# Kernel optimization log

Hardware: AMD Instinct MI355X
Metric: run time of the kernel (lower is better)

Reference implementation:

```python
import jax, jax.numpy as jnp
import numpy as np

EMBED_DIM = 1024
NUM_HEADS = 16


def setup_inputs() -> dict:
    key = jax.random.key(0)
    kx, kq, kk, kv, ko = jax.random.split(key, 5)
    B, S, D = 2, 2048, EMBED_DIM
    s = 1.0 / np.sqrt(D)
    return {
        "x": jax.random.normal(kx, (B, S, D), dtype=jnp.float32),
        "Wq": jax.random.normal(kq, (D, D), dtype=jnp.float32) * s,
        "Wk": jax.random.normal(kk, (D, D), dtype=jnp.float32) * s,
        "Wv": jax.random.normal(kv, (D, D), dtype=jnp.float32) * s,
        "Wo": jax.random.normal(ko, (D, D), dtype=jnp.float32) * s,
    }


def reference(x, Wq, Wk, Wv, Wo):
    B, S, D = x.shape
    H = NUM_HEADS
    d_k = D // H
    # QKV projections (nn.Linear applies x @ W.T)
    q = (x @ Wq.T).reshape(B, S, H, d_k).transpose(0, 2, 1, 3)  # [B,H,S,d_k]
    k = (x @ Wk.T).reshape(B, S, H, d_k).transpose(0, 2, 1, 3)
    v = (x @ Wv.T).reshape(B, S, H, d_k).transpose(0, 2, 1, 3)
    scores = jnp.einsum("bhqd,bhkd->bhqk", q, k) / jnp.sqrt(jnp.float32(d_k))
    probs = jax.nn.softmax(scores, axis=-1)  # dropout is identity in eval
    attn = jnp.einsum("bhqk,bhkd->bhqd", probs, v)  # [B,H,S,d_k]
    attn = attn.transpose(0, 2, 1, 3).reshape(B, S, D)
    return attn @ Wo.T
```

## Files before the change

kernel.cpp:

```cpp
#include <hip/hip_runtime.h>
#include <stdint.h>

typedef __attribute__((ext_vector_type(4))) float    f32x4;
typedef __attribute__((ext_vector_type(8))) _Float16 half8;
typedef __attribute__((ext_vector_type(4))) _Float16 half4;

#define MFMA16(a, b, c)   __builtin_amdgcn_mfma_f32_16x16x32_f16(a, b, c, 0, 0, 0)
#define MFMA16K16(a, b, c) __builtin_amdgcn_mfma_f32_16x16x16f16(a, b, c, 0, 0, 0)

#if __has_builtin(__builtin_amdgcn_exp2f)
#define EXP2F(x) __builtin_amdgcn_exp2f(x)
#else
#define EXP2F(x) exp2f(x)
#endif

#define CEXP 0.18033688f

__device__ inline void gl_lds16(const void* g, void* l) {
    __builtin_amdgcn_global_load_lds(
        (const __attribute__((address_space(1))) unsigned int*)g,
        (__attribute__((address_space(3))) unsigned int*)l, 16, 0, 0);
}

__global__ __launch_bounds__(256) void cast_all(
    const float* __restrict__ x,  const float* __restrict__ wq,
    const float* __restrict__ wk, const float* __restrict__ wv,
    const float* __restrict__ wo,
    _Float16* __restrict__ xh,  _Float16* __restrict__ wqh,
    _Float16* __restrict__ wkh, _Float16* __restrict__ wvh,
    _Float16* __restrict__ woh) {
    const int NX = 4194304, NW = 1048576;
    int i = (blockIdx.x * 256 + threadIdx.x) * 4;
    const float* src; _Float16* dst; int off;
    if (i < NX) { src = x; dst = xh; off = i; }
    else {
        int j = i - NX; int w = j >> 20; off = j & (NW - 1);
        src = (w == 0) ? wq : (w == 1) ? wk : (w == 2) ? wv : wo;
        dst = (w == 0) ? wqh : (w == 1) ? wkh : (w == 2) ? wvh : woh;
    }
    f32x4 v = *(const f32x4*)(src + off);
    half4 o;
    o.x = (_Float16)v.x; o.y = (_Float16)v.y; o.z = (_Float16)v.z; o.w = (_Float16)v.w;
    *(half4*)(dst + off) = o;
}

#define BN 128
#define BK 64

template <int MODE>
__global__ __launch_bounds__(256) void gemm_bt(const _Float16* __restrict__ A,
                                               const _Float16* __restrict__ B,
                                               void* __restrict__ C0,
                                               void* __restrict__ C1,
                                               void* __restrict__ C2,
                                               int M, int N, int K) {
    constexpr int BM  = (MODE == 3) ? 128 : 64;
    constexpr int MT  = BM / 32;
    constexpr int AIT = BM / 32;

    __shared__ __attribute__((aligned(16))) _Float16 As[BM * BK];
    __shared__ __attribute__((aligned(16))) _Float16 Bs[BN * BK];

    const int tid  = threadIdx.x;
    const int wave = tid >> 6;
    const int lane = tid & 63;
    const int l16  = lane & 15;
    const int quad = lane >> 4;
    const int m0 = blockIdx.y * BM;
    const int n0 = blockIdx.x * BN;
    const int wm = (wave >> 1) * (BM / 2);
    const int wn = (wave & 1) * 64;

    const int srow = tid >> 3;
    const int scc  = (tid & 7) ^ ((tid >> 3) & 7);

    f32x4 acc[MT][4];
#pragma unroll
    for (int i = 0; i < MT; i++)
#pragma unroll
        for (int j = 0; j < 4; j++) acc[i][j] = (f32x4){0.f, 0.f, 0.f, 0.f};

    for (int k0 = 0; k0 < K; k0 += BK) {
        __syncthreads();
#pragma unroll
        for (int i = 0; i < AIT; i++)
            gl_lds16(A + (size_t)(m0 + i * 32 + srow) * K + k0 + scc * 8,
                     (char*)As + i * 4096 + wave * 1024);
#pragma unroll
        for (int i = 0; i < 4; i++)
            gl_lds16(B + (size_t)(n0 + i * 32 + srow) * K + k0 + scc * 8,
                     (char*)Bs + i * 4096 + wave * 1024);
        __syncthreads();

#pragma unroll
        for (int kk = 0; kk < 2; kk++) {
            half8 af[MT], bf[4];
#pragma unroll
            for (int mt = 0; mt < MT; mt++) {
                int row = wm + mt * 16 + l16;
                af[mt] = *(const half8*)(As + row * 64 + ((quad + 4 * kk) ^ (row & 7)) * 8);
            }
#pragma unroll
            for (int nt = 0; nt < 4; nt++) {
                int row = wn + nt * 16 + l16;
                bf[nt] = *(const half8*)(Bs + row * 64 + ((quad + 4 * kk) ^ (row & 7)) * 8);
            }
#pragma unroll
            for (int mt = 0; mt < MT; mt++)
#pragma unroll
                for (int nt = 0; nt < 4; nt++)
                    acc[mt][nt] = MFMA16(af[mt], bf[nt], acc[mt][nt]);
        }
    }

    if (MODE == 0) {
        float* C = (float*)C0;
#pragma unroll
        for (int mt = 0; mt < MT; mt++)
#pragma unroll
            for (int r = 0; r < 4; r++) {
                int row = m0 + wm + mt * 16 + quad * 4 + r;
                float* Crow = C + (size_t)row * N + n0 + wn + l16;
#pragma unroll
                for (int nt = 0; nt < 4; nt++) Crow[nt * 16] = acc[mt][nt][r];
            }
    } else {
        const int region = n0 >> 10;
        const int nb = (n0 & 1023) + wn;
        if (region < 2) {
            _Float16* C = (region == 0) ? (_Float16*)C0 : (_Float16*)C1;
#pragma unroll
            for (int mt = 0; mt < MT; mt++)
#pragma unroll
                for (int r = 0; r < 4; r++) {
                    int mg = m0 + wm + mt * 16 + quad * 4 + r;
                    int b = mg >> 11, s = mg & 2047;
#pragma unroll
                    for (int nt = 0; nt < 4; nt++) {
                        int nw = nb + nt * 16 + l16;
                        int h = nw >> 6, d = nw & 63;
                        C[(((size_t)b * 16 + h) * 2048 + s) * 64 + d] = (_Float16)acc[mt][nt][r];
                    }
                }
        } else {
            _Float16* C = (_Float16*)C2;
#pragma unroll
            for (int mt = 0; mt < MT; mt++) {
                int mg = m0 + wm + mt * 16 + quad * 4;
                int b = mg >> 11, s = mg & 2047;
#pragma unroll
                for (int nt = 0; nt < 4; nt++) {
                    int nw = nb + nt * 16 + l16;
                    int h = nw >> 6, d = nw & 63;
                    half4 o;
#pragma unroll
                    for (int r = 0; r < 4; r++) o[r] = (_Float16)acc[mt][nt][r];
                    *(half4*)(C + (((size_t)b * 16 + h) * 64 + d) * 2048 + s) = o;
                }
            }
        }
    }
}

__global__ __launch_bounds__(256) void attn_kernel(const _Float16* __restrict__ Q,
                                                   const _Float16* __restrict__ Kg,
                                                   const _Float16* __restrict__ Vt,
                                                   _Float16* __restrict__ Oa) {
    __shared__ __attribute__((aligned(16))) _Float16 Ks[64 * 64];
    __shared__ __attribute__((aligned(16))) _Float16 Vs[64 * 64];

    const int tid  = threadIdx.x;
    const int wave = tid >> 6;
    const int lane = tid & 63;
    const int l16  = lane & 15;
    const int quad = lane >> 4;
    const int bh = blockIdx.y;
    const int q0 = blockIdx.x * 128 + wave * 32;

    half8 qf[2][2];
#pragma unroll
    for (int qt = 0; qt < 2; qt++)
#pragma unroll
        for (int kk = 0; kk < 2; kk++)
            qf[qt][kk] = *(const half8*)(Q + ((size_t)bh * 2048 + q0 + qt * 16 + l16) * 64 +
                                         (quad + 4 * kk) * 8);

    const _Float16* Kbase = Kg + (size_t)bh * 2048 * 64;
    const _Float16* Vbase = Vt + (size_t)bh * 64 * 2048;

    float lsum[2] = {0.f, 0.f};
    f32x4 oacc[2][4];
#pragma unroll
    for (int qt = 0; qt < 2; qt++)
#pragma unroll
        for (int dt = 0; dt < 4; dt++) oacc[qt][dt] = (f32x4){0.f, 0.f, 0.f, 0.f};

    const int srow = tid >> 3;
    const int scc  = (tid & 7) ^ ((tid >> 3) & 7);

    for (int kt = 0; kt < 2048; kt += 64) {
        __syncthreads();
#pragma unroll
        for (int i = 0; i < 2; i++) {
            int row = i * 32 + srow;
            gl_lds16(Kbase + (size_t)(kt + row) * 64 + scc * 8,
                     (char*)Ks + i * 4096 + wave * 1024);
            gl_lds16(Vbase + (size_t)row * 2048 + kt + scc * 8,
                     (char*)Vs + i * 4096 + wave * 1024);
        }
        __syncthreads();

        f32x4 sc4[2][4];
#pragma unroll
        for (int nt = 0; nt < 4; nt++) {
            int row = nt * 16 + l16;
            half8 kf0 = *(const half8*)(Ks + row * 64 + (quad ^ (row & 7)) * 8);
            half8 kf1 = *(const half8*)(Ks + row * 64 + ((quad + 4) ^ (row & 7)) * 8);
#pragma unroll
            for (int qt = 0; qt < 2; qt++) {
                f32x4 s = (f32x4){0.f, 0.f, 0.f, 0.f};
                s = MFMA16(kf0, qf[qt][0], s);
                s = MFMA16(kf1, qf[qt][1], s);
                sc4[qt][nt] = s;
            }
        }

        half4 ph[2][4];
#pragma unroll
        for (int qt = 0; qt < 2; qt++)
#pragma unroll
            for (int nt = 0; nt < 4; nt++) {
                half4 p;
#pragma unroll
                for (int r = 0; r < 4; r++) {
                    float pe = EXP2F(sc4[qt][nt][r] * CEXP);
                    lsum[qt] += pe;
                    p[r] = (_Float16)pe;
                }
                ph[qt][nt] = p;
            }

#pragma unroll
        for (int nt = 0; nt < 4; nt++) {
#pragma unroll
            for (int dt = 0; dt < 4; dt++) {
                int row = dt * 16 + l16;
                int ch = (nt * 2 + (quad >> 1)) ^ (row & 7);
                half4 vf = *(const half4*)(Vs + row * 64 + ch * 8 + (quad & 1) * 4);
#pragma unroll
                for (int qt = 0; qt < 2; qt++)
                    oacc[qt][dt] = MFMA16K16(vf, ph[qt][nt], oacc[qt][dt]);
            }
        }
    }

    const int b = bh >> 4, h = bh & 15;
#pragma unroll
    for (int qt = 0; qt < 2; qt++) {
        float ls = lsum[qt];
        ls += __shfl_xor(ls, 16);
        ls += __shfl_xor(ls, 32);
        float inv = 1.f / ls;
        int q = q0 + qt * 16 + l16;
        _Float16* orow = Oa + ((size_t)b * 2048 + q) * 1024 + h * 64;
#pragma unroll
        for (int dt = 0; dt < 4; dt++) {
            half4 o;
#pragma unroll
            for (int r = 0; r < 4; r++) o[r] = (_Float16)(oacc[qt][dt][r] * inv);
            *(half4*)(orow + dt * 16 + quad * 4) = o;
        }
    }
}

extern "C" void kernel_launch(void* const* d_in, const int* in_sizes, int n_in,
                              void* d_out, int out_size, void* d_ws, size_t ws_size,
                              hipStream_t stream) {
    const float* x  = (const float*)d_in[0];
    const float* Wq = (const float*)d_in[1];
    const float* Wk = (const float*)d_in[2];
    const float* Wv = (const float*)d_in[3];
    const float* Wo = (const float*)d_in[4];
    float* out = (float*)d_out;

    const int NX = 2 * 2048 * 1024;
    const int NW = 1024 * 1024;

    _Float16* ws  = (_Float16*)d_ws;
    _Float16* xh  = ws;
    _Float16* wqh = xh + NX;
    _Float16* wkh = wqh + NW;
    _Float16* wvh = wkh + NW;
    _Float16* woh = wvh + NW;
    _Float16* Qb  = woh + NW;
    _Float16* Kb  = Qb + NX;
    _Float16* Vtb = Kb + NX;
    _Float16* Ab  = Vtb + NX;

    cast_all<<<8192, 256, 0, stream>>>(x, Wq, Wk, Wv, Wo, xh, wqh, wkh, wvh, woh);

    gemm_bt<3><<<dim3(3072 / 128, 4096 / 128), 256, 0, stream>>>(
        xh, wqh, Qb, Kb, Vtb, 4096, 3072, 1024);

    attn_kernel<<<dim3(16, 32), 256, 0, stream>>>(Qb, Kb, Vtb, Ab);

    gemm_bt<0><<<dim3(1024 / 128, 4096 / 64), 256, 0, stream>>>(
        Ab, woh, out, nullptr, nullptr, 4096, 1024, 1024);
}
```

Before: 201.0 us.

## Register-prefetch K/V tiles, fold softmax scale into Q, stage V epilogue via LDS

The attention kernel now loads the next K/V tile into registers while computing the current one, replacing the direct global-to-LDS loads so global latency overlaps compute. V is stored padded (stride 68) instead of XOR-swizzled. The softmax scale is folded into the Q projection epilogue, which removes a multiply per score, and the row sum is split into four accumulators. The V-transpose epilogue of the QKV GEMM is staged through shared memory so the transposed writes become coalesced 16-byte stores. The risks are higher register pressure, extra LDS store instructions in the attention loop, and precision changes from scaling Q before the fp16 cast.

Result: faster. 191.8 us (-4.5%).

```diff
diff --git a/kernel.cpp b/kernel.cpp
--- a/kernel.cpp
+++ b/kernel.cpp
@@ -4,8 +4,9 @@
 typedef __attribute__((ext_vector_type(4))) float    f32x4;
 typedef __attribute__((ext_vector_type(8))) _Float16 half8;
 typedef __attribute__((ext_vector_type(4))) _Float16 half4;
-
-#define MFMA16(a, b, c)   __builtin_amdgcn_mfma_f32_16x16x32_f16(a, b, c, 0, 0, 0)
+typedef unsigned long long u64;
+
+#define MFMA16(a, b, c)    __builtin_amdgcn_mfma_f32_16x16x32_f16(a, b, c, 0, 0, 0)
 #define MFMA16K16(a, b, c) __builtin_amdgcn_mfma_f32_16x16x16f16(a, b, c, 0, 0, 0)
 
 #if __has_builtin(__builtin_amdgcn_exp2f)
@@ -58,8 +59,9 @@
     constexpr int MT  = BM / 32;
     constexpr int AIT = BM / 32;
 
-    __shared__ __attribute__((aligned(16))) _Float16 As[BM * BK];
-    __shared__ __attribute__((aligned(16))) _Float16 Bs[BN * BK];
+    __shared__ __attribute__((aligned(16))) _Float16 smem[(BM + BN) * BK];
+    _Float16* As = smem;
+    _Float16* Bs = smem + BM * BK;
 
     const int tid  = threadIdx.x;
     const int wave = tid >> 6;
@@ -129,6 +131,7 @@
         const int nb = (n0 & 1023) + wn;
         if (region < 2) {
             _Float16* C = (region == 0) ? (_Float16*)C0 : (_Float16*)C1;
+            const float scale = (region == 0) ? CEXP : 1.f;
 #pragma unroll
             for (int mt = 0; mt < MT; mt++)
 #pragma unroll
@@ -139,24 +142,35 @@
                     for (int nt = 0; nt < 4; nt++) {
                         int nw = nb + nt * 16 + l16;
                         int h = nw >> 6, d = nw & 63;
-                        C[(((size_t)b * 16 + h) * 2048 + s) * 64 + d] = (_Float16)acc[mt][nt][r];
+                        C[(((size_t)b * 16 + h) * 2048 + s) * 64 + d] =
+                            (_Float16)(acc[mt][nt][r] * scale);
                     }
                 }
         } else {
-            _Float16* C = (_Float16*)C2;
-#pragma unroll
-            for (int mt = 0; mt < MT; mt++) {
-                int mg = m0 + wm + mt * 16 + quad * 4;
-                int b = mg >> 11, s = mg & 2047;
+            __syncthreads();
+            _Float16* ep = smem + wave * 4096;
+#pragma unroll
+            for (int mt = 0; mt < MT; mt++)
 #pragma unroll
                 for (int nt = 0; nt < 4; nt++) {
-                    int nw = nb + nt * 16 + l16;
-                    int h = nw >> 6, d = nw & 63;
-                    half4 o;
-#pragma unroll
-                    for (int r = 0; r < 4; r++) o[r] = (_Float16)acc[mt][nt][r];
-                    *(half4*)(C + (((size_t)b * 16 + h) * 64 + d) * 2048 + s) = o;
+                    int dn = nt * 16 + l16;
+                    int slot = (mt * 2 + (quad >> 1)) ^ (dn & 7);
+                    union { half4 h; u64 q; } o;
+#pragma unroll
+                    for (int r = 0; r < 4; r++) o.h[r] = (_Float16)acc[mt][nt][r];
+                    *(u64*)(ep + dn * 64 + slot * 8 + (quad & 1) * 4) = o.q;
                 }
+            __syncthreads();
+            int mgb = m0 + wm;
+            int b = mgb >> 11, sbase = mgb & 2047;
+            int h = nb >> 6;
+            _Float16* C = (_Float16*)C2 + ((size_t)b * 16 + h) * 64 * 2048;
+#pragma unroll
+            for (int j = 0; j < 8; j++) {
+                int dn = j * 8 + (lane >> 3);
+                int slot = (lane & 7) ^ (dn & 7);
+                half8 val = *(const half8*)(ep + dn * 64 + slot * 8);
+                *(half8*)(C + (size_t)dn * 2048 + sbase + (lane & 7) * 8) = val;
             }
         }
     }
@@ -167,7 +181,7 @@
                                                    const _Float16* __restrict__ Vt,
                                                    _Float16* __restrict__ Oa) {
     __shared__ __attribute__((aligned(16))) _Float16 Ks[64 * 64];
-    __shared__ __attribute__((aligned(16))) _Float16 Vs[64 * 64];
+    __shared__ __attribute__((aligned(16))) _Float16 Vs[64 * 68];
 
     const int tid  = threadIdx.x;
     const int wave = tid >> 6;
@@ -185,30 +199,48 @@
             qf[qt][kk] = *(const half8*)(Q + ((size_t)bh * 2048 + q0 + qt * 16 + l16) * 64 +
                                          (quad + 4 * kk) * 8);
 
-    const _Float16* Kbase = Kg + (size_t)bh * 2048 * 64;
-    const _Float16* Vbase = Vt + (size_t)bh * 64 * 2048;
-
-    float lsum[2] = {0.f, 0.f};
+    const int srow = tid >> 3;
+    const int sc8  = tid & 7;
+    const int kslot = sc8 ^ (srow & 7);
+
+    const _Float16* kp = Kg + (size_t)bh * 2048 * 64 + (size_t)srow * 64 + sc8 * 8;
+    const _Float16* vp = Vt + (size_t)bh * 64 * 2048 + (size_t)srow * 2048 + sc8 * 8;
+
+    f32x4 lsum4[2];
     f32x4 oacc[2][4];
 #pragma unroll
-    for (int qt = 0; qt < 2; qt++)
+    for (int qt = 0; qt < 2; qt++) {
+        lsum4[qt] = (f32x4){0.f, 0.f, 0.f, 0.f};
 #pragma unroll
         for (int dt = 0; dt < 4; dt++) oacc[qt][dt] = (f32x4){0.f, 0.f, 0.f, 0.f};
-
-    const int srow = tid >> 3;
-    const int scc  = (tid & 7) ^ ((tid >> 3) & 7);
+    }
+
+    half8 kr0 = *(const half8*)(kp);
+    half8 kr1 = *(const half8*)(kp + 32 * 64);
+    half8 vr0 = *(const half8*)(vp);
+    half8 vr1 = *(const half8*)(vp + 32 * 2048);
 
     for (int kt = 0; kt < 2048; kt += 64) {
         __syncthreads();
-#pragma unroll
-        for (int i = 0; i < 2; i++) {
-            int row = i * 32 + srow;
-            gl_lds16(Kbase + (size_t)(kt + row) * 64 + scc * 8,
-                     (char*)Ks + i * 4096 + wave * 1024);
-            gl_lds16(Vbase + (size_t)row * 2048 + kt + scc * 8,
-                     (char*)Vs + i * 4096 + wave * 1024);
+        *(half8*)(Ks + srow * 64 + kslot * 8) = kr0;
+        *(half8*)(Ks + (srow + 32) * 64 + kslot * 8) = kr1;
+        {
+            union { half8 h; u64 q[2]; } u0, u1;
+            u0.h = vr0; u1.h = vr1;
+            _Float16* vd0 = Vs + srow * 68 + sc8 * 8;
+            _Float16* vd1 = Vs + (srow + 32) * 68 + sc8 * 8;
+            *(u64*)(vd0) = u0.q[0]; *(u64*)(vd0 + 4) = u0.q[1];
+            *(u64*)(vd1) = u1.q[0]; *(u64*)(vd1 + 4) = u1.q[1];
         }
         __syncthreads();
+
+        {
+            int kt2 = (kt + 64) & 2047;
+            kr0 = *(const half8*)(kp + (size_t)kt2 * 64);
+            kr1 = *(const half8*)(kp + (size_t)(kt2 + 32) * 64);
+            vr0 = *(const half8*)(vp + kt2);
+            vr1 = *(const half8*)(vp + 32 * 2048 + kt2);
+        }
 
         f32x4 sc4[2][4];
 #pragma unroll
@@ -233,8 +265,8 @@
                 half4 p;
 #pragma unroll
                 for (int r = 0; r < 4; r++) {
-                    float pe = EXP2F(sc4[qt][nt][r] * CEXP);
-                    lsum[qt] += pe;
+                    float pe = EXP2F(sc4[qt][nt][r]);
+                    lsum4[qt][r] += pe;
                     p[r] = (_Float16)pe;
                 }
                 ph[qt][nt] = p;
@@ -245,8 +277,7 @@
 #pragma unroll
             for (int dt = 0; dt < 4; dt++) {
                 int row = dt * 16 + l16;
-                int ch = (nt * 2 + (quad >> 1)) ^ (row & 7);
-                half4 vf = *(const half4*)(Vs + row * 64 + ch * 8 + (quad & 1) * 4);
+                half4 vf = *(const half4*)(Vs + row * 68 + nt * 16 + quad * 4);
 #pragma unroll
                 for (int qt = 0; qt < 2; qt++)
                     oacc[qt][dt] = MFMA16K16(vf, ph[qt][nt], oacc[qt][dt]);
@@ -257,7 +288,7 @@
     const int b = bh >> 4, h = bh & 15;
 #pragma unroll
     for (int qt = 0; qt < 2; qt++) {
-        float ls = lsum[qt];
+        float ls = (lsum4[qt][0] + lsum4[qt][1]) + (lsum4[qt][2] + lsum4[qt][3]);
         ls += __shfl_xor(ls, 16);
         ls += __shfl_xor(ls, 32);
         float inv = 1.f / ls;
```
